# Optimization experiments

Hardware: AMD Instinct MI355X
Metric: run time of the kernel (lower is better)

The kernel has to match this reference:

```python
import jax, jax.numpy as jnp
import numpy as np

N, M, K, D = 8192, 64, 256, 16  # n_vecs, subvector_num, ksub (2**subvector_bits), dsub


def setup_inputs() -> dict:
    key = jax.random.key(0)
    k1, k2 = jax.random.split(key)
    vecs = jax.random.normal(k1, (N, M * D), dtype=jnp.float32)
    codebook = jax.random.normal(k2, (M, K, D), dtype=jnp.float32)
    return {"vecs": vecs, "codebook": codebook}


def reference(vecs, codebook):
    # quantization pipeline: code_selection -> get_index -> quantized_vecs
    n = vecs.shape[0]
    m, k, d = codebook.shape
    v = vecs.reshape(n, m, d)
    # proba = -||v - c||^2 computed via expansion (same math, no [N,M,K,D] broadcast)
    v2 = jnp.sum(v * v, axis=-1)[:, :, None]            # [N,M,1]
    c2 = jnp.sum(codebook * codebook, axis=-1)[None]    # [1,M,K]
    vc = jnp.einsum('nmd,mkd->nmk', v, codebook)        # [N,M,K]
    proba = -(v2 - 2.0 * vc + c2)
    # softmax is monotonic -> argmax(softmax(proba)) == argmax(proba)
    index = jnp.argmax(proba, axis=-1)                  # [N,M] int
    # quantized_vecs: one-hot scatter + matmul == gather of selected codewords
    quantized = codebook[jnp.arange(m)[None, :], index] # [N,M,D]
    return quantized.reshape(n, m * d)
```

## Files before the change

### kernel.cpp

```cpp
#include <hip/hip_runtime.h>
#include <math.h>

#define M_SUB 64
#define K_CODES 256
#define D_DIM 16
#define ROW_F 1024
#define THRGAP 0.0078125f
#define SLICE_B 17408

typedef __attribute__((ext_vector_type(8))) short short8;
typedef __attribute__((ext_vector_type(4))) float f32x4;

__device__ inline unsigned bfr(float x) {
    unsigned u = __builtin_bit_cast(unsigned, x);
    return (u + 0x7FFFu + ((u >> 16) & 1u)) >> 16;
}
__device__ inline float bff(unsigned h) { return __builtin_bit_cast(float, h << 16); }

template <int C> __device__ inline float dppf(float x) {
    return __builtin_bit_cast(float,
        __builtin_amdgcn_update_dpp(0, __builtin_bit_cast(int, x), C, 0xF, 0xF, true));
}
template <int C> __device__ inline int dppi(int x) {
    return __builtin_amdgcn_update_dpp(0, x, C, 0xF, 0xF, true);
}

__global__ __launch_bounds__(256) void pq_convert_kernel(
    const float* __restrict__ cb, char* __restrict__ pk)
{
    const int m = blockIdx.x, k = threadIdx.x;
    const float* cp = cb + ((size_t)m * K_CODES + k) * D_DIM;
    float f[16];
    #pragma unroll
    for (int q = 0; q < 4; ++q) {
        float4 t4 = ((const float4*)cp)[q];
        f[q*4+0] = t4.x; f[q*4+1] = t4.y; f[q*4+2] = t4.z; f[q*4+3] = t4.w;
    }
    float c2 = 0.f;
    #pragma unroll
    for (int d = 0; d < 16; ++d) c2 = fmaf(f[d], f[d], c2);
    short hi[16], lo[16];
    #pragma unroll
    for (int d = 0; d < 16; ++d) {
        unsigned h = bfr(f[d]);
        hi[d] = (short)h;
        lo[d] = (short)bfr(f[d] - bff(h));
    }
    char* sb = pk + (size_t)m * SLICE_B;
    *(float*)(sb + k * 4) = -c2;
    char* tb = sb + 1024 + (k >> 4) * 1024;
    const int lr = k & 15;
    short8 v0 = { hi[0],hi[1],hi[2],hi[3],hi[4],hi[5],hi[6],hi[7] };
    short8 v1 = { hi[8],hi[9],hi[10],hi[11],hi[12],hi[13],hi[14],hi[15] };
    short8 v2 = { lo[0],lo[1],lo[2],lo[3],lo[4],lo[5],lo[6],lo[7] };
    short8 v3 = { lo[8],lo[9],lo[10],lo[11],lo[12],lo[13],lo[14],lo[15] };
    *(short8*)(tb +   0 + lr * 16) = v0;
    *(short8*)(tb + 256 + lr * 16) = v1;
    *(short8*)(tb + 512 + lr * 16) = v2;
    *(short8*)(tb + 768 + lr * 16) = v3;
}

__global__ __launch_bounds__(256, 4) void pq_mfma_kernel(
    const float* __restrict__ vecs, const float* __restrict__ cb,
    float* __restrict__ out, const char* __restrict__ pk)
{
    const int tid  = threadIdx.x;
    const int w    = tid >> 6;
    const int lane = tid & 63;
    const int lr   = lane & 15;
    const int lg   = lane >> 4;
    const int wid  = blockIdx.x * 4 + w;
    const int m    = wid >> 9;
    const int n0   = (wid & 511) * 16;

    __shared__ unsigned IDXW[4][4];
    __shared__ unsigned FLGW[4][4];

    const char* pkm = pk + (size_t)m * SLICE_B;

    float nc2v[16];
    #pragma unroll
    for (int kt = 0; kt < 16; ++kt)
        nc2v[kt] = *(const float*)(pkm + (kt * 16 + lr) * 4);

    const float* vp = vecs + (size_t)(n0 + lr) * ROW_F + m * D_DIM + (lg & 1) * 8;
    float4 a4 = ((const float4*)vp)[0];
    float4 b4 = ((const float4*)vp)[1];
    float f[8];
    f[0]=2.f*a4.x; f[1]=2.f*a4.y; f[2]=2.f*a4.z; f[3]=2.f*a4.w;
    f[4]=2.f*b4.x; f[5]=2.f*b4.y; f[6]=2.f*b4.z; f[7]=2.f*b4.w;
    short hi[8], lo[8];
    #pragma unroll
    for (int e = 0; e < 8; ++e) {
        unsigned h = bfr(f[e]);
        hi[e] = (short)h;
        lo[e] = (short)bfr(f[e] - bff(h));
    }
    short8 H = { hi[0],hi[1],hi[2],hi[3],hi[4],hi[5],hi[6],hi[7] };
    short8 L = { lo[0],lo[1],lo[2],lo[3],lo[4],lo[5],lo[6],lo[7] };
    const bool hiSide = (lg < 2);
    short8 A1 = hiSide ? H : L;
    short8 A2 = hiSide ? L : H;

    f32x4 acc[16];
    #pragma unroll
    for (int kt = 0; kt < 16; ++kt) {
        short8 B = *(const short8*)(pkm + 1024 + kt * 1024 + lane * 16);
        float nv = nc2v[kt];
        f32x4 c0 = { nv, nv, nv, nv };
        c0 = __builtin_amdgcn_mfma_f32_16x16x32_bf16(A1, B, c0, 0, 0, 0);
        c0 = __builtin_amdgcn_mfma_f32_16x16x32_bf16(A2, B, c0, 0, 0, 0);
        acc[kt] = c0;
    }

    {
        unsigned kp[4]; unsigned rf = 0;
        #pragma unroll
        for (int p = 0; p < 4; ++p) {
            float x0 = fmaxf(fmaxf(acc[0][p],  acc[1][p]),  acc[2][p]);
            float x1 = fmaxf(fmaxf(acc[3][p],  acc[4][p]),  acc[5][p]);
            float x2 = fmaxf(fmaxf(acc[6][p],  acc[7][p]),  acc[8][p]);
            float x3 = fmaxf(fmaxf(acc[9][p],  acc[10][p]), acc[11][p]);
            float x4 = fmaxf(fmaxf(acc[12][p], acc[13][p]), acc[14][p]);
            float b  = fmaxf(fmaxf(fmaxf(x0, x1), x2), fmaxf(fmaxf(x3, x4), acc[15][p]));
            b = fmaxf(b, dppf<0xB1>(b));
            b = fmaxf(b, dppf<0x4E>(b));
            b = fmaxf(b, dppf<0x141>(b));
            b = fmaxf(b, dppf<0x140>(b));
            const float bthr = b - THRGAP;
            unsigned Mm = 0;
            #pragma unroll
            for (int kt = 15; kt >= 0; --kt)
                Mm = Mm + Mm + (acc[kt][p] >= bthr ? 1u : 0u);
            int cl  = __popc(Mm);
            int bkt = __ffs(Mm) - 1;
            int bkv = Mm ? (bkt * 16 + lr) : 0x7FFFFFFF;
            cl += dppi<0xB1>(cl);  bkv = min(bkv, dppi<0xB1>(bkv));
            cl += dppi<0x4E>(cl);  bkv = min(bkv, dppi<0x4E>(bkv));
            cl += dppi<0x141>(cl); bkv = min(bkv, dppi<0x141>(bkv));
            cl += dppi<0x140>(cl); bkv = min(bkv, dppi<0x140>(bkv));
            if (bkv > 255) bkv = 0;
            kp[p] = (unsigned)bkv;
            rf |= (cl != 1) ? (1u << p) : 0u;
        }
        if (lr == 0) {
            IDXW[w][lg] = kp[0] | (kp[1] << 8) | (kp[2] << 16) | (kp[3] << 24);
            FLGW[w][lg] = rf;
        }
    }

    #pragma unroll 1
    for (int e = 0; e < 4; ++e) {
        unsigned rf = FLGW[w][e];
        if (rf) {
            #pragma unroll 1
            for (int p = 0; p < 4; ++p) if (rf & (1u << p)) {
                const int n = n0 + e * 4 + p;
                const float* vrow = vecs + (size_t)n * ROW_F + m * D_DIM;
                double vd[16];
                #pragma unroll
                for (int d = 0; d < 16; ++d) vd[d] = (double)vrow[d];
                double bs = -1e300; int bi = 0;
                #pragma unroll
                for (int j = 0; j < 4; ++j) {
                    int k = lane * 4 + j;
                    const float* cp = cb + ((size_t)m * K_CODES + k) * D_DIM;
                    double vc = 0.0, c2 = 0.0;
                    #pragma unroll
                    for (int d = 0; d < 16; ++d) {
                        double cd = (double)cp[d];
                        vc = fma(vd[d], cd, vc);
                        c2 = fma(cd, cd, c2);
                    }
                    double s = 2.0 * vc - c2;
                    if (s > bs) { bs = s; bi = k; }
                }
                #pragma unroll
                for (int off = 32; off; off >>= 1) {
                    double so = __shfl_xor(bs, off, 64);
                    int    ko = __shfl_xor(bi, off, 64);
                    if (so > bs || (so == bs && ko < bi)) { bs = so; bi = ko; }
                }
                if (lane == 0) ((char*)&IDXW[w][e])[p] = (char)bi;
            }
        }
    }

    {
        const int r = lane >> 2;
        unsigned e4 = IDXW[w][r >> 2];
        const int k = (int)((e4 >> ((r & 3) * 8)) & 255u);
        const float4* src = (const float4*)(cb + ((size_t)m * K_CODES + k) * D_DIM);
        float4 val = src[lane & 3];
        float4* dst = (float4*)(out + (size_t)(n0 + r) * ROW_F + m * D_DIM);
        dst[lane & 3] = val;
    }
}

extern "C" void kernel_launch(void* const* d_in, const int* in_sizes, int n_in,
                              void* d_out, int out_size, void* d_ws, size_t ws_size,
                              hipStream_t stream) {
    const float* vecs = (const float*)d_in[0];
    const float* cb   = (const float*)d_in[1];
    float* out        = (float*)d_out;
    char* pk          = (char*)d_ws;

    pq_convert_kernel<<<M_SUB, 256, 0, stream>>>(cb, pk);
    pq_mfma_kernel<<<8192, 256, 0, stream>>>(vecs, cb, out, pk);
}
```

Measured before the change: 60.84 us.

## Stage packed codebook slice in LDS and loop each wave over multiple row tiles

```diff
diff --git a/kernel.cpp b/kernel.cpp
--- a/kernel.cpp
+++ b/kernel.cpp
@@ -7,6 +7,7 @@
 #define ROW_F 1024
 #define THRGAP 0.0078125f
 #define SLICE_B 17408
+#define NT 8
 
 typedef __attribute__((ext_vector_type(8))) short short8;
 typedef __attribute__((ext_vector_type(4))) float f32x4;
@@ -47,9 +48,9 @@
         lo[d] = (short)bfr(f[d] - bff(h));
     }
     char* sb = pk + (size_t)m * SLICE_B;
-    *(float*)(sb + k * 4) = -c2;
-    char* tb = sb + 1024 + (k >> 4) * 1024;
-    const int lr = k & 15;
+    const int kt = k >> 4, lr = k & 15;
+    *(float*)(sb + ((lr * 16) + kt) * 4) = -c2;
+    char* tb = sb + 1024 + kt * 1024;
     short8 v0 = { hi[0],hi[1],hi[2],hi[3],hi[4],hi[5],hi[6],hi[7] };
     short8 v1 = { hi[8],hi[9],hi[10],hi[11],hi[12],hi[13],hi[14],hi[15] };
     short8 v2 = { lo[0],lo[1],lo[2],lo[3],lo[4],lo[5],lo[6],lo[7] };
@@ -69,131 +70,153 @@
     const int lane = tid & 63;
     const int lr   = lane & 15;
     const int lg   = lane >> 4;
-    const int wid  = blockIdx.x * 4 + w;
-    const int m    = wid >> 9;
-    const int n0   = (wid & 511) * 16;
-
+    const int m    = blockIdx.x >> 4;
+    const int q    = (blockIdx.x & 15) * 4 + w;
+    const int nbase = q * (NT * 16);
+
+    __shared__ __align__(16) char BL[SLICE_B];
     __shared__ unsigned IDXW[4][4];
     __shared__ unsigned FLGW[4][4];
 
     const char* pkm = pk + (size_t)m * SLICE_B;
 
-    float nc2v[16];
-    #pragma unroll
-    for (int kt = 0; kt < 16; ++kt)
-        nc2v[kt] = *(const float*)(pkm + (kt * 16 + lr) * 4);
-
-    const float* vp = vecs + (size_t)(n0 + lr) * ROW_F + m * D_DIM + (lg & 1) * 8;
-    float4 a4 = ((const float4*)vp)[0];
-    float4 b4 = ((const float4*)vp)[1];
-    float f[8];
-    f[0]=2.f*a4.x; f[1]=2.f*a4.y; f[2]=2.f*a4.z; f[3]=2.f*a4.w;
-    f[4]=2.f*b4.x; f[5]=2.f*b4.y; f[6]=2.f*b4.z; f[7]=2.f*b4.w;
-    short hi[8], lo[8];
-    #pragma unroll
-    for (int e = 0; e < 8; ++e) {
-        unsigned h = bfr(f[e]);
-        hi[e] = (short)h;
-        lo[e] = (short)bfr(f[e] - bff(h));
-    }
-    short8 H = { hi[0],hi[1],hi[2],hi[3],hi[4],hi[5],hi[6],hi[7] };
-    short8 L = { lo[0],lo[1],lo[2],lo[3],lo[4],lo[5],lo[6],lo[7] };
-    const bool hiSide = (lg < 2);
-    short8 A1 = hiSide ? H : L;
-    short8 A2 = hiSide ? L : H;
-
-    f32x4 acc[16];
-    #pragma unroll
-    for (int kt = 0; kt < 16; ++kt) {
-        short8 B = *(const short8*)(pkm + 1024 + kt * 1024 + lane * 16);
-        float nv = nc2v[kt];
-        f32x4 c0 = { nv, nv, nv, nv };
-        c0 = __builtin_amdgcn_mfma_f32_16x16x32_bf16(A1, B, c0, 0, 0, 0);
-        c0 = __builtin_amdgcn_mfma_f32_16x16x32_bf16(A2, B, c0, 0, 0, 0);
-        acc[kt] = c0;
-    }
-
-    {
-        unsigned kp[4]; unsigned rf = 0;
+    const float* vbase = vecs + (size_t)(nbase + lr) * ROW_F + m * D_DIM + (lg & 1) * 8;
+    float4 curA0 = ((const float4*)vbase)[0];
+    float4 curA1 = ((const float4*)vbase)[1];
+
+    f32x4 nq[4];
+    nq[0] = *(const f32x4*)(pkm + lr * 64 +  0);
+    nq[1] = *(const f32x4*)(pkm + lr * 64 + 16);
+    nq[2] = *(const f32x4*)(pkm + lr * 64 + 32);
+    nq[3] = *(const f32x4*)(pkm + lr * 64 + 48);
+
+    for (int c = tid * 16; c < SLICE_B; c += 256 * 16) {
+        *(float4*)(BL + c) = *(const float4*)(pkm + c);
+    }
+    __syncthreads();
+
+    #pragma unroll 1
+    for (int it = 0; it < NT; ++it) {
+        float4 nxtA0 = curA0, nxtA1 = curA1;
+        if (it + 1 < NT) {
+            const float* vn = vbase + (size_t)(it + 1) * 16 * ROW_F;
+            nxtA0 = ((const float4*)vn)[0];
+            nxtA1 = ((const float4*)vn)[1];
+        }
+
+        float f[8];
+        f[0]=2.f*curA0.x; f[1]=2.f*curA0.y; f[2]=2.f*curA0.z; f[3]=2.f*curA0.w;
+        f[4]=2.f*curA1.x; f[5]=2.f*curA1.y; f[6]=2.f*curA1.z; f[7]=2.f*curA1.w;
+        short hi[8], lo[8];
         #pragma unroll
-        for (int p = 0; p < 4; ++p) {
-            float x0 = fmaxf(fmaxf(acc[0][p],  acc[1][p]),  acc[2][p]);
-            float x1 = fmaxf(fmaxf(acc[3][p],  acc[4][p]),  acc[5][p]);
-            float x2 = fmaxf(fmaxf(acc[6][p],  acc[7][p]),  acc[8][p]);
-            float x3 = fmaxf(fmaxf(acc[9][p],  acc[10][p]), acc[11][p]);
-            float x4 = fmaxf(fmaxf(acc[12][p], acc[13][p]), acc[14][p]);
-            float b  = fmaxf(fmaxf(fmaxf(x0, x1), x2), fmaxf(fmaxf(x3, x4), acc[15][p]));
-            b = fmaxf(b, dppf<0xB1>(b));
-            b = fmaxf(b, dppf<0x4E>(b));
-            b = fmaxf(b, dppf<0x141>(b));
-            b = fmaxf(b, dppf<0x140>(b));
-            const float bthr = b - THRGAP;
-            unsigned Mm = 0;
+        for (int e = 0; e < 8; ++e) {
+            unsigned h = bfr(f[e]);
+            hi[e] = (short)h;
+            lo[e] = (short)bfr(f[e] - bff(h));
+        }
+        short8 H = { hi[0],hi[1],hi[2],hi[3],hi[4],hi[5],hi[6],hi[7] };
+        short8 L = { lo[0],lo[1],lo[2],lo[3],lo[4],lo[5],lo[6],lo[7] };
+        const bool hiSide = (lg < 2);
+        short8 A1 = hiSide ? H : L;
+        short8 A2 = hiSide ? L : H;
+
+        f32x4 acc[16];
+        #pragma unroll
+        for (int kt = 0; kt < 16; ++kt) {
+            short8 B = *(const short8*)(BL + 1024 + kt * 1024 + lane * 16);
+            float nv = nq[kt >> 2][kt & 3];
+            f32x4 c0 = { nv, nv, nv, nv };
+            c0 = __builtin_amdgcn_mfma_f32_16x16x32_bf16(A1, B, c0, 0, 0, 0);
+            c0 = __builtin_amdgcn_mfma_f32_16x16x32_bf16(A2, B, c0, 0, 0, 0);
+            acc[kt] = c0;
+        }
+
+        {
+            unsigned kp[4]; unsigned rf = 0;
             #pragma unroll
-            for (int kt = 15; kt >= 0; --kt)
-                Mm = Mm + Mm + (acc[kt][p] >= bthr ? 1u : 0u);
-            int cl  = __popc(Mm);
-            int bkt = __ffs(Mm) - 1;
-            int bkv = Mm ? (bkt * 16 + lr) : 0x7FFFFFFF;
-            cl += dppi<0xB1>(cl);  bkv = min(bkv, dppi<0xB1>(bkv));
-            cl += dppi<0x4E>(cl);  bkv = min(bkv, dppi<0x4E>(bkv));
-            cl += dppi<0x141>(cl); bkv = min(bkv, dppi<0x141>(bkv));
-            cl += dppi<0x140>(cl); bkv = min(bkv, dppi<0x140>(bkv));
-            if (bkv > 255) bkv = 0;
-            kp[p] = (unsigned)bkv;
-            rf |= (cl != 1) ? (1u << p) : 0u;
-        }
-        if (lr == 0) {
-            IDXW[w][lg] = kp[0] | (kp[1] << 8) | (kp[2] << 16) | (kp[3] << 24);
-            FLGW[w][lg] = rf;
-        }
-    }
-
-    #pragma unroll 1
-    for (int e = 0; e < 4; ++e) {
-        unsigned rf = FLGW[w][e];
-        if (rf) {
-            #pragma unroll 1
-            for (int p = 0; p < 4; ++p) if (rf & (1u << p)) {
-                const int n = n0 + e * 4 + p;
-                const float* vrow = vecs + (size_t)n * ROW_F + m * D_DIM;
-                double vd[16];
+            for (int p = 0; p < 4; ++p) {
+                float x0 = fmaxf(fmaxf(acc[0][p],  acc[1][p]),  acc[2][p]);
+                float x1 = fmaxf(fmaxf(acc[3][p],  acc[4][p]),  acc[5][p]);
+                float x2 = fmaxf(fmaxf(acc[6][p],  acc[7][p]),  acc[8][p]);
+                float x3 = fmaxf(fmaxf(acc[9][p],  acc[10][p]), acc[11][p]);
+                float x4 = fmaxf(fmaxf(acc[12][p], acc[13][p]), acc[14][p]);
+                float b  = fmaxf(fmaxf(fmaxf(x0, x1), x2), fmaxf(fmaxf(x3, x4), acc[15][p]));
+                b = fmaxf(b, dppf<0xB1>(b));
+                b = fmaxf(b, dppf<0x4E>(b));
+                b = fmaxf(b, dppf<0x141>(b));
+                b = fmaxf(b, dppf<0x140>(b));
+                const float bthr = b - THRGAP;
+                unsigned Mm = 0;
                 #pragma unroll
-                for (int d = 0; d < 16; ++d) vd[d] = (double)vrow[d];
-                double bs = -1e300; int bi = 0;
-                #pragma unroll
-                for (int j = 0; j < 4; ++j) {
-                    int k = lane * 4 + j;
-                    const float* cp = cb + ((size_t)m * K_CODES + k) * D_DIM;
-                    double vc = 0.0, c2 = 0.0;
+                for (int kt = 15; kt >= 0; --kt)
+                    Mm = Mm + Mm + (acc[kt][p] >= bthr ? 1u : 0u);
+                int cl  = __popc(Mm);
+                int bkt = __ffs(Mm) - 1;
+                int bkv = Mm ? (bkt * 16 + lr) : 0x7FFFFFFF;
+                cl += dppi<0xB1>(cl);  bkv = min(bkv, dppi<0xB1>(bkv));
+                cl += dppi<0x4E>(cl);  bkv = min(bkv, dppi<0x4E>(bkv));
+                cl += dppi<0x141>(cl); bkv = min(bkv, dppi<0x141>(bkv));
+                cl += dppi<0x140>(cl); bkv = min(bkv, dppi<0x140>(bkv));
+                if (bkv > 255) bkv = 0;
+                kp[p] = (unsigned)bkv;
+                rf |= (cl != 1) ? (1u << p) : 0u;
+            }
+            if (lr == 0) {
+                IDXW[w][lg] = kp[0] | (kp[1] << 8) | (kp[2] << 16) | (kp[3] << 24);
+                FLGW[w][lg] = rf;
+            }
+        }
+
+        const int n0 = nbase + it * 16;
+
+        #pragma unroll 1
+        for (int e = 0; e < 4; ++e) {
+            unsigned rf = FLGW[w][e];
+            if (rf) {
+                #pragma unroll 1
+                for (int p = 0; p < 4; ++p) if (rf & (1u << p)) {
+                    const int n = n0 + e * 4 + p;
+                    const float* vrow = vecs + (size_t)n * ROW_F + m * D_DIM;
+                    double vd[16];
                     #pragma unroll
-                    for (int d = 0; d < 16; ++d) {
-                        double cd = (double)cp[d];
-                        vc = fma(vd[d], cd, vc);
-                        c2 = fma(cd, cd, c2);
+                    for (int d = 0; d < 16; ++d) vd[d] = (double)vrow[d];
+                    double bs = -1e300; int bi = 0;
+                    #pragma unroll
+                    for (int j = 0; j < 4; ++j) {
+                        int k = lane * 4 + j;
+                        const float* cp = cb + ((size_t)m * K_CODES + k) * D_DIM;
+                        double vc = 0.0, c2 = 0.0;
+                        #pragma unroll
+                        for (int d = 0; d < 16; ++d) {
+                            double cd = (double)cp[d];
+                            vc = fma(vd[d], cd, vc);
+                            c2 = fma(cd, cd, c2);
+                        }
+                        double s = 2.0 * vc - c2;
+                        if (s > bs) { bs = s; bi = k; }
                     }
-                    double s = 2.0 * vc - c2;
-                    if (s > bs) { bs = s; bi = k; }
+                    #pragma unroll
+                    for (int off = 32; off; off >>= 1) {
+                        double so = __shfl_xor(bs, off, 64);
+                        int    ko = __shfl_xor(bi, off, 64);
+                        if (so > bs || (so == bs && ko < bi)) { bs = so; bi = ko; }
+                    }
+                    if (lane == 0) ((char*)&IDXW[w][e])[p] = (char)bi;
                 }
-                #pragma unroll
-                for (int off = 32; off; off >>= 1) {
-                    double so = __shfl_xor(bs, off, 64);
-                    int    ko = __shfl_xor(bi, off, 64);
-                    if (so > bs || (so == bs && ko < bi)) { bs = so; bi = ko; }
-                }
-                if (lane == 0) ((char*)&IDXW[w][e])[p] = (char)bi;
             }
         }
-    }
-
-    {
-        const int r = lane >> 2;
-        unsigned e4 = IDXW[w][r >> 2];
-        const int k = (int)((e4 >> ((r & 3) * 8)) & 255u);
-        const float4* src = (const float4*)(cb + ((size_t)m * K_CODES + k) * D_DIM);
-        float4 val = src[lane & 3];
-        float4* dst = (float4*)(out + (size_t)(n0 + r) * ROW_F + m * D_DIM);
-        dst[lane & 3] = val;
+
+        {
+            const int r = lane >> 2;
+            unsigned e4 = IDXW[w][r >> 2];
+            const int k = (int)((e4 >> ((r & 3) * 8)) & 255u);
+            const float4* src = (const float4*)(cb + ((size_t)m * K_CODES + k) * D_DIM);
+            float4 val = src[lane & 3];
+            float4* dst = (float4*)(out + (size_t)(n0 + r) * ROW_F + m * D_DIM);
+            dst[lane & 3] = val;
+        }
+
+        curA0 = nxtA0; curA1 = nxtA1;
     }
 }
 
@@ -206,5 +229,5 @@
     char* pk          = (char*)d_ws;
 
     pq_convert_kernel<<<M_SUB, 256, 0, stream>>>(cb, pk);
-    pq_mfma_kernel<<<8192, 256, 0, stream>>>(vecs, cb, out, pk);
-}
+    pq_mfma_kernel<<<1024, 256, 0, stream>>>(vecs, cb, out, pk);
+}
```

Result: slower. 179.4 us (+194.9%).

## Interleave codeword norms into tiles, stagger tile order per wave, use 1024-thread blocks

Applied to the files above, without the earlier changes.

```diff
diff --git a/kernel.cpp b/kernel.cpp
--- a/kernel.cpp
+++ b/kernel.cpp
@@ -6,7 +6,8 @@
 #define D_DIM 16
 #define ROW_F 1024
 #define THRGAP 0.0078125f
-#define SLICE_B 17408
+#define TILE_B 1088
+#define SLICE_B (16 * TILE_B)
 
 typedef __attribute__((ext_vector_type(8))) short short8;
 typedef __attribute__((ext_vector_type(4))) float f32x4;
@@ -46,9 +47,7 @@
         hi[d] = (short)h;
         lo[d] = (short)bfr(f[d] - bff(h));
     }
-    char* sb = pk + (size_t)m * SLICE_B;
-    *(float*)(sb + k * 4) = -c2;
-    char* tb = sb + 1024 + (k >> 4) * 1024;
+    char* tb = pk + (size_t)m * SLICE_B + (k >> 4) * TILE_B;
     const int lr = k & 15;
     short8 v0 = { hi[0],hi[1],hi[2],hi[3],hi[4],hi[5],hi[6],hi[7] };
     short8 v1 = { hi[8],hi[9],hi[10],hi[11],hi[12],hi[13],hi[14],hi[15] };
@@ -58,9 +57,10 @@
     *(short8*)(tb + 256 + lr * 16) = v1;
     *(short8*)(tb + 512 + lr * 16) = v2;
     *(short8*)(tb + 768 + lr * 16) = v3;
-}
-
-__global__ __launch_bounds__(256, 4) void pq_mfma_kernel(
+    *(float*)(tb + 1024 + lr * 4) = -c2;
+}
+
+__global__ __launch_bounds__(1024) void pq_mfma_kernel(
     const float* __restrict__ vecs, const float* __restrict__ cb,
     float* __restrict__ out, const char* __restrict__ pk)
 {
@@ -69,19 +69,15 @@
     const int lane = tid & 63;
     const int lr   = lane & 15;
     const int lg   = lane >> 4;
-    const int wid  = blockIdx.x * 4 + w;
+    const int wid  = blockIdx.x * 16 + w;
     const int m    = wid >> 9;
     const int n0   = (wid & 511) * 16;
-
-    __shared__ unsigned IDXW[4][4];
-    __shared__ unsigned FLGW[4][4];
+    const int off  = w & 15;
+
+    __shared__ unsigned IDXW[16][4];
+    __shared__ unsigned FLGW[16][4];
 
     const char* pkm = pk + (size_t)m * SLICE_B;
-
-    float nc2v[16];
-    #pragma unroll
-    for (int kt = 0; kt < 16; ++kt)
-        nc2v[kt] = *(const float*)(pkm + (kt * 16 + lr) * 4);
 
     const float* vp = vecs + (size_t)(n0 + lr) * ROW_F + m * D_DIM + (lg & 1) * 8;
     float4 a4 = ((const float4*)vp)[0];
@@ -104,13 +100,15 @@
 
     f32x4 acc[16];
     #pragma unroll
-    for (int kt = 0; kt < 16; ++kt) {
-        short8 B = *(const short8*)(pkm + 1024 + kt * 1024 + lane * 16);
-        float nv = nc2v[kt];
+    for (int i = 0; i < 16; ++i) {
+        const int ktp = (i + off) & 15;
+        const char* tb = pkm + ktp * TILE_B;
+        short8 B = *(const short8*)(tb + lane * 16);
+        float nv = *(const float*)(tb + 1024 + lr * 4);
         f32x4 c0 = { nv, nv, nv, nv };
         c0 = __builtin_amdgcn_mfma_f32_16x16x32_bf16(A1, B, c0, 0, 0, 0);
         c0 = __builtin_amdgcn_mfma_f32_16x16x32_bf16(A2, B, c0, 0, 0, 0);
-        acc[kt] = c0;
+        acc[i] = c0;
     }
 
     {
@@ -130,10 +128,11 @@
             const float bthr = b - THRGAP;
             unsigned Mm = 0;
             #pragma unroll
-            for (int kt = 15; kt >= 0; --kt)
-                Mm = Mm + Mm + (acc[kt][p] >= bthr ? 1u : 0u);
+            for (int i = 15; i >= 0; --i)
+                Mm = Mm + Mm + (acc[i][p] >= bthr ? 1u : 0u);
+            unsigned Ml = ((Mm << off) | (Mm >> (16 - off))) & 0xFFFFu;
             int cl  = __popc(Mm);
-            int bkt = __ffs(Mm) - 1;
+            int bkt = __ffs(Ml) - 1;
             int bkv = Mm ? (bkt * 16 + lr) : 0x7FFFFFFF;
             cl += dppi<0xB1>(cl);  bkv = min(bkv, dppi<0xB1>(bkv));
             cl += dppi<0x4E>(cl);  bkv = min(bkv, dppi<0x4E>(bkv));
@@ -176,9 +175,9 @@
                     if (s > bs) { bs = s; bi = k; }
                 }
                 #pragma unroll
-                for (int off = 32; off; off >>= 1) {
-                    double so = __shfl_xor(bs, off, 64);
-                    int    ko = __shfl_xor(bi, off, 64);
+                for (int offr = 32; offr; offr >>= 1) {
+                    double so = __shfl_xor(bs, offr, 64);
+                    int    ko = __shfl_xor(bi, offr, 64);
                     if (so > bs || (so == bs && ko < bi)) { bs = so; bi = ko; }
                 }
                 if (lane == 0) ((char*)&IDXW[w][e])[p] = (char)bi;
@@ -206,5 +205,5 @@
     char* pk          = (char*)d_ws;
 
     pq_convert_kernel<<<M_SUB, 256, 0, stream>>>(cb, pk);
-    pq_mfma_kernel<<<8192, 256, 0, stream>>>(vecs, cb, out, pk);
-}
+    pq_mfma_kernel<<<2048, 1024, 0, stream>>>(vecs, cb, out, pk);
+}
```

Result: slower. 72.24 us (+18.7%).
